# Kernel optimization log

Hardware: AMD Instinct MI355X
Metric: run time of the kernel (lower is better)

## Reference

```python
import jax, jax.numpy as jnp
from jax import lax
import numpy as np

B, T, H, E = 4096, 16, 1024, 1024


def setup_inputs() -> dict:
    key = jax.random.key(0)
    ks = jax.random.split(key, 6)
    query = jax.random.normal(ks[0], (B, H), dtype=jnp.float32)
    topics = jax.random.normal(ks[1], (B, T, E), dtype=jnp.float32)
    coverage_vector = jax.random.uniform(ks[2], (B, T), dtype=jnp.float32)
    # Ua: Linear(embed->hidden, bias=False); weight [H, E]
    Ua_w = jax.random.normal(ks[3], (H, E), dtype=jnp.float32) * 0.03
    # Wa: Linear(hidden->hidden, bias=False). Applied repeatedly (T times) to
    # query in the original loop, so keep spectral norm < 1 for stability.
    Wa_w = jax.random.normal(ks[4], (H, H), dtype=jnp.float32) * 0.01
    # va: Linear(hidden->1, bias=True)
    va_w = jax.random.normal(ks[5], (1, H), dtype=jnp.float32) * 0.03
    va_b = jnp.zeros((1,), dtype=jnp.float32)
    return {"query": query, "topics": topics, "coverage_vector": coverage_vector,
            "Ua_w": Ua_w, "Wa_w": Wa_w, "va_w": va_w, "va_b": va_b}


def reference(query, topics, coverage_vector, Ua_w, Wa_w, va_w, va_b):
    # proj_key for all steps at once: Ua(topics[:, i, :]) -> [B, T, H]
    proj_keys = jnp.einsum('bte,he->bth', topics, Ua_w)
    # Original loop mutates query = Wa(query) each step, so step i uses
    # Wa^(i+1) @ query. Sequential dependence -> lax.scan over T.
    def step(q, pk_c):
        pk, c = pk_c                       # pk: [B, H], c: [B]
        q = q @ Wa_w.T                     # query = Wa(query)
        s = (jnp.tanh(q + pk) @ va_w.T)[:, 0] + va_b[0]  # va(tanh(.)) -> [B]
        return q, s * c                    # scale by coverage C_t[:, i]
    xs = (jnp.swapaxes(proj_keys, 0, 1), coverage_vector.T)  # [T,B,H], [T,B]
    _, scores = lax.scan(step, query, xs)  # scores: [T, B]
    scores = scores.T                      # [B, T]
    alphas = jax.nn.softmax(scores, axis=1)
    mt = jnp.einsum('bt,bte->be', alphas, topics)  # bmm(alphas[:,None,:], topics)
    return mt, alphas
```

## Files before the change

kernel.cpp:

```cpp
#include <hip/hip_runtime.h>

typedef unsigned short u16;
typedef unsigned int u32;
typedef __attribute__((ext_vector_type(8))) __bf16 bf16x8;
typedef __attribute__((ext_vector_type(4))) float f32x4;

__device__ __forceinline__ u16 f2bf(float f) {
  u32 u = __float_as_uint(f);
  u32 r = (u + 0x7FFFu + ((u >> 16) & 1u)) >> 16;
  return (u16)r;
}

__device__ __forceinline__ void gload_lds16(const void* g, void* l) {
  __builtin_amdgcn_global_load_lds((const __attribute__((address_space(1))) u32*)g,
                                   (__attribute__((address_space(3))) u32*)l, 16, 0, 0);
}

__device__ __forceinline__ float fast_tanh(float x) {
  x = fminf(fmaxf(x, -15.f), 15.f);
  float e2 = __expf(2.f * x);
  return (e2 - 1.f) / (e2 + 1.f);
}

__global__ __launch_bounds__(256) void cvt_kernel(const float* __restrict__ src,
                                                  u16* __restrict__ dst, int n4) {
  int stride = gridDim.x * blockDim.x;
  for (int i = blockIdx.x * blockDim.x + threadIdx.x; i < n4; i += stride) {
    float4 v = reinterpret_cast<const float4*>(src)[i];
    ushort4 o;
    o.x = f2bf(v.x); o.y = f2bf(v.y); o.z = f2bf(v.z); o.w = f2bf(v.w);
    reinterpret_cast<ushort4*>(dst)[i] = o;
  }
}

__global__ __launch_bounds__(256) void cvt3t_kernel(const float* __restrict__ q_src, u16* __restrict__ q_dst,
                                                    const float* __restrict__ u_src, u16* __restrict__ u_dst,
                                                    const float* __restrict__ w_src, u16* __restrict__ w_dst,
                                                    u16* __restrict__ wt_dst) {
  __shared__ float tile[32][33];
  int b = blockIdx.x;
  if (b < 6144) {
    const float* src; u16* dst; int i;
    if (b < 4096)      { src = q_src; dst = q_dst; i = b * 256 + threadIdx.x; }
    else if (b < 5120) { src = u_src; dst = u_dst; i = (b - 4096) * 256 + threadIdx.x; }
    else               { src = w_src; dst = w_dst; i = (b - 5120) * 256 + threadIdx.x; }
    float4 v = reinterpret_cast<const float4*>(src)[i];
    ushort4 o;
    o.x = f2bf(v.x); o.y = f2bf(v.y); o.z = f2bf(v.z); o.w = f2bf(v.w);
    reinterpret_cast<ushort4*>(dst)[i] = o;
  } else {
    int tb = b - 6144;
    int tx = threadIdx.x & 31, ty = threadIdx.x >> 5;
    int bx = (tb & 31) * 32, by = (tb >> 5) * 32;
#pragma unroll
    for (int j = 0; j < 32; j += 8)
      tile[ty + j][tx] = w_src[(size_t)(by + ty + j) * 1024 + bx + tx];
    __syncthreads();
#pragma unroll
    for (int j = 0; j < 32; j += 8)
      wt_dst[(size_t)(bx + ty + j) * 1024 + by + tx] = f2bf(tile[tx][ty + j]);
  }
}

__device__ __forceinline__ void stage_tile(const u16* __restrict__ g, size_t row_stride,
                                           u16* lds, int tid) {
#pragma unroll
  for (int s = 0; s < 4; ++s) {
    int chunk = s * 256 + tid;
    int row = chunk >> 3;
    int kcl = (chunk & 7) ^ (row & 7);
    const u16* gp = g + (size_t)row * row_stride + (size_t)(kcl * 8);
    u16* lp = lds + (tid >> 6) * 512 + s * 2048;
    gload_lds16(gp, lp);
  }
}

struct PowArgs {
  const u16* A[8];
  const u16* Bt[8];
  u16* C[8];
  u16* Ct[8];
};

__global__ __launch_bounds__(256) void pow_gemm_kernel(PowArgs args) {
  const u16* A  = args.A[blockIdx.z];
  const u16* Bt = args.Bt[blockIdx.z];
  u16* C  = args.C[blockIdx.z];
  u16* Ct = args.Ct[blockIdx.z];

  __shared__ __align__(16) u16 As[8192];
  __shared__ __align__(16) u16 Bs[8192];

  int tid = threadIdx.x;
  int lane = tid & 63, wave = tid >> 6;
  int wr = wave >> 1, wc = wave & 1;
  int lr = lane & 15, lg = lane >> 4;
  int m0 = blockIdx.x * 128, n0 = blockIdx.y * 128;

  f32x4 acc[4][4];
  const f32x4 zero = {0.f, 0.f, 0.f, 0.f};
#pragma unroll
  for (int m = 0; m < 4; ++m)
#pragma unroll
    for (int n = 0; n < 4; ++n) acc[m][n] = zero;

  for (int k0 = 0; k0 < 1024; k0 += 64) {
    stage_tile(A + (size_t)m0 * 1024 + k0, 1024, As, tid);
    stage_tile(Bt + (size_t)n0 * 1024 + k0, 1024, Bs, tid);
    __syncthreads();
#pragma unroll
    for (int ks = 0; ks < 2; ++ks) {
      bf16x8 a[4], b[4];
#pragma unroll
      for (int m = 0; m < 4; ++m) {
        int ra = wr * 64 + m * 16 + lr;
        a[m] = *reinterpret_cast<const bf16x8*>(As + ra * 64 + (((ks * 4 + lg) ^ (ra & 7)) << 3));
      }
#pragma unroll
      for (int n = 0; n < 4; ++n) {
        int rb = wc * 64 + n * 16 + lr;
        b[n] = *reinterpret_cast<const bf16x8*>(Bs + rb * 64 + (((ks * 4 + lg) ^ (rb & 7)) << 3));
      }
#pragma unroll
      for (int m = 0; m < 4; ++m)
#pragma unroll
        for (int n = 0; n < 4; ++n)
          acc[m][n] = __builtin_amdgcn_mfma_f32_16x16x32_bf16(a[m], b[n], acc[m][n], 0, 0, 0);
    }
    __syncthreads();
  }

#pragma unroll
  for (int m = 0; m < 4; ++m) {
    int row0 = m0 + wr * 64 + m * 16 + lg * 4;
#pragma unroll
    for (int n = 0; n < 4; ++n) {
      int col = n0 + wc * 64 + n * 16 + lr;
      f32x4 c = acc[m][n];
      ushort4 pk;
      pk.x = f2bf(c[0]); pk.y = f2bf(c[1]); pk.z = f2bf(c[2]); pk.w = f2bf(c[3]);
      C[(size_t)(row0 + 0) * 1024 + col] = pk.x;
      C[(size_t)(row0 + 1) * 1024 + col] = pk.y;
      C[(size_t)(row0 + 2) * 1024 + col] = pk.z;
      C[(size_t)(row0 + 3) * 1024 + col] = pk.w;
      *reinterpret_cast<ushort4*>(Ct + (size_t)col * 1024 + row0) = pk;
    }
  }
}

__device__ __forceinline__ void stage_tile64(const u16* __restrict__ g, u16* lds, int tid) {
#pragma unroll
  for (int s = 0; s < 2; ++s) {
    int chunk = s * 256 + tid;
    int row = chunk >> 3;
    int kcl = (chunk & 7) ^ (row & 7);
    const u16* gp = g + (size_t)row * 1024 + (size_t)(kcl * 8);
    u16* lp = lds + (tid >> 6) * 512 + s * 2048;
    gload_lds16(gp, lp);
  }
}

__global__ __launch_bounds__(256) void pow64_gemm_kernel(PowArgs args) {
  const u16* A  = args.A[blockIdx.z];
  const u16* Bt = args.Bt[blockIdx.z];
  u16* C  = args.C[blockIdx.z];
  u16* Ct = args.Ct[blockIdx.z];

  __shared__ __align__(16) u16 As[4096];
  __shared__ __align__(16) u16 Bs[4096];

  int tid = threadIdx.x;
  int lane = tid & 63, wave = tid >> 6;
  int wr = wave >> 1, wc = wave & 1;
  int lr = lane & 15, lg = lane >> 4;
  int m0 = blockIdx.x * 64, n0 = blockIdx.y * 64;

  f32x4 acc[2][2];
  const f32x4 zero = {0.f, 0.f, 0.f, 0.f};
#pragma unroll
  for (int m = 0; m < 2; ++m)
#pragma unroll
    for (int n = 0; n < 2; ++n) acc[m][n] = zero;

  for (int k0 = 0; k0 < 1024; k0 += 64) {
    stage_tile64(A + (size_t)m0 * 1024 + k0, As, tid);
    stage_tile64(Bt + (size_t)n0 * 1024 + k0, Bs, tid);
    __syncthreads();
#pragma unroll
    for (int ks = 0; ks < 2; ++ks) {
      bf16x8 a[2], b[2];
#pragma unroll
      for (int m = 0; m < 2; ++m) {
        int ra = wr * 32 + m * 16 + lr;
        a[m] = *reinterpret_cast<const bf16x8*>(As + ra * 64 + (((ks * 4 + lg) ^ (ra & 7)) << 3));
      }
#pragma unroll
      for (int n = 0; n < 2; ++n) {
        int rb = wc * 32 + n * 16 + lr;
        b[n] = *reinterpret_cast<const bf16x8*>(Bs + rb * 64 + (((ks * 4 + lg) ^ (rb & 7)) << 3));
      }
#pragma unroll
      for (int m = 0; m < 2; ++m)
#pragma unroll
        for (int n = 0; n < 2; ++n)
          acc[m][n] = __builtin_amdgcn_mfma_f32_16x16x32_bf16(a[m], b[n], acc[m][n], 0, 0, 0);
    }
    __syncthreads();
  }

#pragma unroll
  for (int m = 0; m < 2; ++m) {
    int row0 = m0 + wr * 32 + m * 16 + lg * 4;
#pragma unroll
    for (int n = 0; n < 2; ++n) {
      int col = n0 + wc * 32 + n * 16 + lr;
      f32x4 c = acc[m][n];
      ushort4 pk;
      pk.x = f2bf(c[0]); pk.y = f2bf(c[1]); pk.z = f2bf(c[2]); pk.w = f2bf(c[3]);
      C[(size_t)(row0 + 0) * 1024 + col] = pk.x;
      C[(size_t)(row0 + 1) * 1024 + col] = pk.y;
      C[(size_t)(row0 + 2) * 1024 + col] = pk.z;
      C[(size_t)(row0 + 3) * 1024 + col] = pk.w;
      *reinterpret_cast<ushort4*>(Ct + (size_t)col * 1024 + row0) = pk;
    }
  }
}


#define QPHASE(CUR, KS, STAGE_STMT, WAIT_STMT)                                        \
  { _Pragma("unroll") for (int m_ = 0; m_ < 8; ++m_)                                  \
      af[m_] = *reinterpret_cast<const bf16x8*>(lds + aoffv[m_] +                     \
                                                (CUR)*32768 + (KS)*16384);            \
    _Pragma("unroll") for (int n_ = 0; n_ < 4; ++n_)                                  \
      bfr[n_] = *reinterpret_cast<const bf16x8*>(lds + boffv[n_] +                    \
                                                 (CUR)*32768 + (KS)*16384);           \
    STAGE_STMT;                                                                       \
    __builtin_amdgcn_s_barrier();                                                     \
    asm volatile("s_waitcnt lgkmcnt(0)" ::: "memory");                                \
    __builtin_amdgcn_sched_barrier(0);                                                \
    __builtin_amdgcn_s_setprio(1);                                                    \
    _Pragma("unroll") for (int m_ = 0; m_ < 8; ++m_)                                  \
      _Pragma("unroll") for (int n_ = 0; n_ < 4; ++n_)                                \
        acc[m_][n_] =                                                                 \
            __builtin_amdgcn_mfma_f32_16x16x32_bf16(af[m_], bfr[n_], acc[m_][n_], 0, 0, 0); \
    __builtin_amdgcn_s_setprio(0);                                                    \
    WAIT_STMT;                                                                        \
    __builtin_amdgcn_s_barrier();                                                     \
    __builtin_amdgcn_sched_barrier(0); }

__global__ __launch_bounds__(512, 2) void score8_kernel(
    const u16* __restrict__ query_bf, const u16* __restrict__ topics_bf,
    const u16* __restrict__ F_base, const u16* __restrict__ Ua_bf,
    const float* __restrict__ va_w, float* __restrict__ scores_part) {
  extern __shared__ __align__(16) char lds[];

  const int tid = threadIdx.x;
  const int lane = tid & 63, wave = tid >> 6;
  const int wm = wave >> 2, wn = wave & 3;
  const int lr = lane & 15, lg = lane >> 4;

  const int bid = blockIdx.x;
  const int lid = (bid & 7) * 128 + (bid >> 3);
  const int x = lid & 15, y = (lid >> 4) & 3, t = lid >> 6;
  const int m0 = x * 256, n0 = y * 256;
  const int NT = 32;

  const u16* Ft = F_base + (size_t)t * (1024 * 1024);

  u32 aoffv[8], boffv[4];
#pragma unroll
  for (int m = 0; m < 8; ++m) {
    int row = wm * 128 + m * 16 + lr;
    aoffv[m] = row * 64 + ((lg ^ ((row >> 1) & 3)) << 4);
  }
#pragma unroll
  for (int n = 0; n < 4; ++n) {
    int row = wn * 64 + n * 16 + lr;
    boffv[n] = 65536 + row * 64 + ((lg ^ ((row >> 1) & 3)) << 4);
  }

  u32 goff1[2], goff2[2];
#pragma unroll
  for (int s = 0; s < 2; ++s) {
    int c = s * 512 + tid;
    int row = c >> 2;
    int cl = (c & 3) ^ ((row >> 1) & 3);
    goff1[s] = row * 1024 + cl * 8;
    goff2[s] = row * 16384 + cl * 8;
  }
  char* sdst = lds + (tid >> 6) * 1024;
  const u16* qbase = query_bf + (size_t)m0 * 1024;
  const u16* tbase = topics_bf + (size_t)m0 * 16384 + (size_t)t * 1024 - 1024;
  const u16* fbase = Ft + (size_t)n0 * 1024;
  const u16* ubase = Ua_bf + (size_t)n0 * 1024 - 1024;

  auto stageA = [&](int kt, int ks, int buf) {
    const u16* base = (kt < 16 ? qbase : tbase) + kt * 64 + ks * 32;
#pragma unroll
    for (int s = 0; s < 2; ++s) {
      u32 off = (kt < 16) ? goff1[s] : goff2[s];
      gload_lds16(base + off, sdst + buf * 32768 + ks * 16384 + s * 8192);
    }
  };
  auto stageB = [&](int kt, int ks, int buf) {
    const u16* base = (kt < 16 ? fbase : ubase) + kt * 64 + ks * 32;
#pragma unroll
    for (int s = 0; s < 2; ++s)
      gload_lds16(base + goff1[s], sdst + 65536 + buf * 32768 + ks * 16384 + s * 8192);
  };

  f32x4 acc[8][4];
  const f32x4 zero = {0.f, 0.f, 0.f, 0.f};
#pragma unroll
  for (int m = 0; m < 8; ++m)
#pragma unroll
    for (int n = 0; n < 4; ++n) acc[m][n] = zero;

  bf16x8 af[8], bfr[4];

  stageA(0, 0, 0); stageB(0, 0, 0);
  stageA(0, 1, 0); stageB(0, 1, 0);
  stageA(1, 0, 1); stageB(1, 0, 1);
  asm volatile("s_waitcnt vmcnt(4)" ::: "memory");
  __builtin_amdgcn_s_barrier();
  __builtin_amdgcn_sched_barrier(0);

#pragma unroll 2
  for (int kt = 0; kt < NT; ++kt) {
    int cur = kt & 1, nxt = cur ^ 1;
    QPHASE(cur, 0,
           { if (kt + 1 < NT) { stageA(kt + 1, 1, nxt); stageB(kt + 1, 1, nxt); } },
           {});
    QPHASE(cur, 1,
           { if (kt + 2 < NT) { stageA(kt + 2, 0, cur); stageB(kt + 2, 0, cur); } },
           { if (kt < NT - 2)       { asm volatile("s_waitcnt vmcnt(4)" ::: "memory"); }
             else if (kt == NT - 2) { asm volatile("s_waitcnt vmcnt(0)" ::: "memory"); } });
  }

  float va_c[4];
#pragma unroll
  for (int n = 0; n < 4; ++n) va_c[n] = va_w[n0 + wn * 64 + n * 16 + lr];

  float* sred = (float*)lds;
#pragma unroll
  for (int m = 0; m < 8; ++m) {
    float rs[4] = {0.f, 0.f, 0.f, 0.f};
#pragma unroll
    for (int n = 0; n < 4; ++n) {
      f32x4 c = acc[m][n];
      rs[0] += va_c[n] * fast_tanh(c[0]);
      rs[1] += va_c[n] * fast_tanh(c[1]);
      rs[2] += va_c[n] * fast_tanh(c[2]);
      rs[3] += va_c[n] * fast_tanh(c[3]);
    }
#pragma unroll
    for (int j = 0; j < 4; ++j) {
      float v = rs[j];
      v += __shfl_xor(v, 1);
      v += __shfl_xor(v, 2);
      v += __shfl_xor(v, 4);
      v += __shfl_xor(v, 8);
      if (lr == 0) sred[wn * 256 + wm * 128 + m * 16 + lg * 4 + j] = v;
    }
  }
  __syncthreads();
  if (tid < 256) {
    float s = sred[tid] + sred[256 + tid] + sred[512 + tid] + sred[768 + tid];
    scores_part[((size_t)y * 4096 + m0 + tid) * 16 + t] = s;
  }
}

__global__ __launch_bounds__(256) void softmax_mt_kernel(
    const float* __restrict__ scores_part, const float* __restrict__ cov,
    const float* __restrict__ topics, const float* __restrict__ va_b,
    float* __restrict__ mt, float* __restrict__ alphas) {
  int b = blockIdx.x;
  int tid = threadIdx.x;
  float vb = va_b[0];
  float e[16];
  float mx = -3.4e38f;
#pragma unroll
  for (int t = 0; t < 16; ++t) {
    float s = 0.f;
#pragma unroll
    for (int yy = 0; yy < 4; ++yy) s += scores_part[((size_t)yy * 4096 + b) * 16 + t];
    s = (s + vb) * cov[b * 16 + t];
    e[t] = s;
    mx = fmaxf(mx, s);
  }
  float sum = 0.f;
#pragma unroll
  for (int t = 0; t < 16; ++t) { e[t] = __expf(e[t] - mx); sum += e[t]; }
  float inv = 1.f / sum;
  if (tid == 0) {
#pragma unroll
    for (int t = 0; t < 16; ++t) alphas[b * 16 + t] = e[t] * inv;
  }
  const float4* tp = reinterpret_cast<const float4*>(topics + (size_t)b * 16384);
  float4 accv = {0.f, 0.f, 0.f, 0.f};
#pragma unroll
  for (int t = 0; t < 16; ++t) {
    float4 v = tp[t * 256 + tid];
    float a = e[t] * inv;
    accv.x += a * v.x; accv.y += a * v.y; accv.z += a * v.z; accv.w += a * v.w;
  }
  reinterpret_cast<float4*>(mt + (size_t)b * 1024)[tid] = accv;
}

extern "C" void kernel_launch(void* const* d_in, const int* in_sizes, int n_in,
                              void* d_out, int out_size, void* d_ws, size_t ws_size,
                              hipStream_t stream) {
  (void)in_sizes; (void)n_in; (void)out_size; (void)ws_size;
  const float* query = (const float*)d_in[0];
  const float* topics = (const float*)d_in[1];
  const float* cov   = (const float*)d_in[2];
  const float* Ua    = (const float*)d_in[3];
  const float* Wa    = (const float*)d_in[4];
  const float* va_w  = (const float*)d_in[5];
  const float* va_b  = (const float*)d_in[6];

  float* mt = (float*)d_out;
  float* alphas = mt + (size_t)4096 * 1024;

  char* ws = (char*)d_ws;
  u16* topics_bf = (u16*)(ws);
  u16* query_bf  = (u16*)(ws + (size_t)128 * 1024 * 1024);
  u16* Ua_bf     = (u16*)(ws + (size_t)136 * 1024 * 1024);
  u16* F_base    = (u16*)(ws + (size_t)138 * 1024 * 1024);
  u16* FT_base   = (u16*)(ws + (size_t)170 * 1024 * 1024);
  float* scores_part = (float*)(ws + (size_t)202 * 1024 * 1024);

  hipFuncSetAttribute(reinterpret_cast<const void*>(score8_kernel),
                      hipFuncAttributeMaxDynamicSharedMemorySize, 131072);

  cvt_kernel<<<8192, 256, 0, stream>>>(topics, topics_bf, 16777216);
  cvt3t_kernel<<<7168, 256, 0, stream>>>(query, query_bf, Ua, Ua_bf, Wa, F_base, FT_base);

  const size_t MS = 1024 * 1024;
  auto F  = [&](int i) { return F_base + (size_t)i * MS; };
  auto FT = [&](int i) { return FT_base + (size_t)i * MS; };

  PowArgs a1{};
  a1.A[0] = F(0); a1.Bt[0] = FT(0); a1.C[0] = F(1); a1.Ct[0] = FT(1);
  pow64_gemm_kernel<<<dim3(16, 16, 1), 256, 0, stream>>>(a1);
  PowArgs a2{};
  a2.A[0] = F(1); a2.Bt[0] = FT(0); a2.C[0] = F(2); a2.Ct[0] = FT(2);
  a2.A[1] = F(1); a2.Bt[1] = FT(1); a2.C[1] = F(3); a2.Ct[1] = FT(3);
  pow64_gemm_kernel<<<dim3(16, 16, 2), 256, 0, stream>>>(a2);
  PowArgs a3{};
  for (int p = 0; p < 4; ++p) { a3.A[p] = F(3); a3.Bt[p] = FT(p); a3.C[p] = F(4 + p); a3.Ct[p] = FT(4 + p); }
  pow_gemm_kernel<<<dim3(8, 8, 4), 256, 0, stream>>>(a3);
  PowArgs a4{};
  for (int p = 0; p < 8; ++p) { a4.A[p] = F(7); a4.Bt[p] = FT(p); a4.C[p] = F(8 + p); a4.Ct[p] = FT(8 + p); }
  pow_gemm_kernel<<<dim3(8, 8, 8), 256, 0, stream>>>(a4);

  score8_kernel<<<1024, 512, 131072, stream>>>(query_bf, topics_bf, F_base, Ua_bf,
                                               va_w, scores_part);
  softmax_mt_kernel<<<4096, 256, 0, stream>>>(scores_part, cov, topics, va_b, mt, alphas);
}
```

Before: 817.6 us.

## Replace high Wa powers with precomputed q·Wa^8 and reuse low powers

Drops the last batch of eight 1024x1024 matrix-power GEMMs. Instead it computes q8 = query·(Wa^8)^T once with a new qgemm kernel, and score steps 8..15 reuse the powers 0..7 applied to q8. The topics conversion is merged into the other conversion kernels as one launch. The score kernel switches to a 3D grid without the blockIdx swizzle, and setprio/sched_barrier and one barrier are removed from its inner loop. This trades the eight power GEMMs for a single 4096x1024x1024 GEMM. It may hurt the score kernel's scheduling and L2 locality, and it adds one more bf16 rounding step on q8.

After: 792.2 us. 3.1% less time.

```diff
diff --git a/kernel.cpp b/kernel.cpp
--- a/kernel.cpp
+++ b/kernel.cpp
@@ -22,34 +22,32 @@
   return (e2 - 1.f) / (e2 + 1.f);
 }
 
-__global__ __launch_bounds__(256) void cvt_kernel(const float* __restrict__ src,
-                                                  u16* __restrict__ dst, int n4) {
-  int stride = gridDim.x * blockDim.x;
-  for (int i = blockIdx.x * blockDim.x + threadIdx.x; i < n4; i += stride) {
-    float4 v = reinterpret_cast<const float4*>(src)[i];
-    ushort4 o;
-    o.x = f2bf(v.x); o.y = f2bf(v.y); o.z = f2bf(v.z); o.w = f2bf(v.w);
-    reinterpret_cast<ushort4*>(dst)[i] = o;
-  }
-}
-
-__global__ __launch_bounds__(256) void cvt3t_kernel(const float* __restrict__ q_src, u16* __restrict__ q_dst,
-                                                    const float* __restrict__ u_src, u16* __restrict__ u_dst,
-                                                    const float* __restrict__ w_src, u16* __restrict__ w_dst,
-                                                    u16* __restrict__ wt_dst) {
+__global__ __launch_bounds__(256) void cvtall_kernel(
+    const float* __restrict__ topics, u16* __restrict__ topics_bf,
+    const float* __restrict__ q_src, u16* __restrict__ q_dst,
+    const float* __restrict__ u_src, u16* __restrict__ u_dst,
+    const float* __restrict__ w_src, u16* __restrict__ w_dst,
+    u16* __restrict__ wt_dst) {
   __shared__ float tile[32][33];
   int b = blockIdx.x;
-  if (b < 6144) {
+  if (b < 8192) {
+    for (int i = b * 256 + threadIdx.x; i < 16777216; i += 8192 * 256) {
+      float4 v = reinterpret_cast<const float4*>(topics)[i];
+      ushort4 o;
+      o.x = f2bf(v.x); o.y = f2bf(v.y); o.z = f2bf(v.z); o.w = f2bf(v.w);
+      reinterpret_cast<ushort4*>(topics_bf)[i] = o;
+    }
+  } else if (b < 14336) {
     const float* src; u16* dst; int i;
-    if (b < 4096)      { src = q_src; dst = q_dst; i = b * 256 + threadIdx.x; }
-    else if (b < 5120) { src = u_src; dst = u_dst; i = (b - 4096) * 256 + threadIdx.x; }
-    else               { src = w_src; dst = w_dst; i = (b - 5120) * 256 + threadIdx.x; }
+    if (b < 12288)      { src = q_src; dst = q_dst; i = (b - 8192) * 256 + threadIdx.x; }
+    else if (b < 13312) { src = u_src; dst = u_dst; i = (b - 12288) * 256 + threadIdx.x; }
+    else                { src = w_src; dst = w_dst; i = (b - 13312) * 256 + threadIdx.x; }
     float4 v = reinterpret_cast<const float4*>(src)[i];
     ushort4 o;
     o.x = f2bf(v.x); o.y = f2bf(v.y); o.z = f2bf(v.z); o.w = f2bf(v.w);
     reinterpret_cast<ushort4*>(dst)[i] = o;
   } else {
-    int tb = b - 6144;
+    int tb = b - 14336;
     int tx = threadIdx.x & 31, ty = threadIdx.x >> 5;
     int bx = (tb & 31) * 32, by = (tb >> 5) * 32;
 #pragma unroll
@@ -148,6 +146,66 @@
   }
 }
 
+__global__ __launch_bounds__(256) void qgemm_kernel(const u16* __restrict__ A,
+                                                    const u16* __restrict__ Bt,
+                                                    u16* __restrict__ C) {
+  __shared__ __align__(16) u16 As[8192];
+  __shared__ __align__(16) u16 Bs[8192];
+
+  int tid = threadIdx.x;
+  int lane = tid & 63, wave = tid >> 6;
+  int wr = wave >> 1, wc = wave & 1;
+  int lr = lane & 15, lg = lane >> 4;
+  int m0 = blockIdx.x * 128, n0 = blockIdx.y * 128;
+
+  f32x4 acc[4][4];
+  const f32x4 zero = {0.f, 0.f, 0.f, 0.f};
+#pragma unroll
+  for (int m = 0; m < 4; ++m)
+#pragma unroll
+    for (int n = 0; n < 4; ++n) acc[m][n] = zero;
+
+  for (int k0 = 0; k0 < 1024; k0 += 64) {
+    stage_tile(A + (size_t)m0 * 1024 + k0, 1024, As, tid);
+    stage_tile(Bt + (size_t)n0 * 1024 + k0, 1024, Bs, tid);
+    __syncthreads();
+#pragma unroll
+    for (int ks = 0; ks < 2; ++ks) {
+      bf16x8 a[4], b[4];
+#pragma unroll
+      for (int m = 0; m < 4; ++m) {
+        int ra = wr * 64 + m * 16 + lr;
+        a[m] = *reinterpret_cast<const bf16x8*>(As + ra * 64 + (((ks * 4 + lg) ^ (ra & 7)) << 3));
+      }
+#pragma unroll
+      for (int n = 0; n < 4; ++n) {
+        int rb = wc * 64 + n * 16 + lr;
+        b[n] = *reinterpret_cast<const bf16x8*>(Bs + rb * 64 + (((ks * 4 + lg) ^ (rb & 7)) << 3));
+      }
+#pragma unroll
+      for (int m = 0; m < 4; ++m)
+#pragma unroll
+        for (int n = 0; n < 4; ++n)
+          acc[m][n] = __builtin_amdgcn_mfma_f32_16x16x32_bf16(a[m], b[n], acc[m][n], 0, 0, 0);
+    }
+    __syncthreads();
+  }
+
+#pragma unroll
+  for (int m = 0; m < 4; ++m) {
+    int row0 = m0 + wr * 64 + m * 16 + lg * 4;
+#pragma unroll
+    for (int n = 0; n < 4; ++n) {
+      int col = n0 + wc * 64 + n * 16 + lr;
+      f32x4 c = acc[m][n];
+      C[(size_t)(row0 + 0) * 1024 + col] = f2bf(c[0]);
+      C[(size_t)(row0 + 1) * 1024 + col] = f2bf(c[1]);
+      C[(size_t)(row0 + 2) * 1024 + col] = f2bf(c[2]);
+      C[(size_t)(row0 + 3) * 1024 + col] = f2bf(c[3]);
+    }
+  }
+}
+
 __device__ __forceinline__ void stage_tile64(const u16* __restrict__ g, u16* lds, int tid) {
 #pragma unroll
   for (int s = 0; s < 2; ++s) {
@@ -235,21 +293,16 @@
       bfr[n_] = *reinterpret_cast<const bf16x8*>(lds + boffv[n_] +                    \
                                                  (CUR)*32768 + (KS)*16384);           \
     STAGE_STMT;                                                                       \
-    __builtin_amdgcn_s_barrier();                                                     \
-    asm volatile("s_waitcnt lgkmcnt(0)" ::: "memory");                                \
-    __builtin_amdgcn_sched_barrier(0);                                                \
-    __builtin_amdgcn_s_setprio(1);                                                    \
     _Pragma("unroll") for (int m_ = 0; m_ < 8; ++m_)                                  \
       _Pragma("unroll") for (int n_ = 0; n_ < 4; ++n_)                                \
         acc[m_][n_] =                                                                 \
             __builtin_amdgcn_mfma_f32_16x16x32_bf16(af[m_], bfr[n_], acc[m_][n_], 0, 0, 0); \
-    __builtin_amdgcn_s_setprio(0);                                                    \
     WAIT_STMT;                                                                        \
-    __builtin_amdgcn_s_barrier();                                                     \
-    __builtin_amdgcn_sched_barrier(0); }
+    __builtin_amdgcn_s_barrier(); }
 
 __global__ __launch_bounds__(512, 2) void score8_kernel(
-    const u16* __restrict__ query_bf, const u16* __restrict__ topics_bf,
+    const u16* __restrict__ query_bf, const u16* __restrict__ q8_bf,
+    const u16* __restrict__ topics_bf,
     const u16* __restrict__ F_base, const u16* __restrict__ Ua_bf,
     const float* __restrict__ va_w, float* __restrict__ scores_part) {
   extern __shared__ __align__(16) char lds[];
@@ -258,14 +311,11 @@
   const int lane = tid & 63, wave = tid >> 6;
   const int wm = wave >> 2, wn = wave & 3;
   const int lr = lane & 15, lg = lane >> 4;
-
-  const int bid = blockIdx.x;
-  const int lid = (bid & 7) * 128 + (bid >> 3);
-  const int x = lid & 15, y = (lid >> 4) & 3, t = lid >> 6;
-  const int m0 = x * 256, n0 = y * 256;
+  const int m0 = blockIdx.x * 256, n0 = blockIdx.y * 256;
+  const int t = blockIdx.z;
   const int NT = 32;
 
-  const u16* Ft = F_base + (size_t)t * (1024 * 1024);
+  const u16* Ft = F_base + (size_t)(t & 7) * (1024 * 1024);
 
   u32 aoffv[8], boffv[4];
 #pragma unroll
@@ -289,7 +339,7 @@
     goff2[s] = row * 16384 + cl * 8;
   }
   char* sdst = lds + (tid >> 6) * 1024;
-  const u16* qbase = query_bf + (size_t)m0 * 1024;
+  const u16* qbase = (t < 8 ? query_bf : q8_bf) + (size_t)m0 * 1024;
   const u16* tbase = topics_bf + (size_t)m0 * 16384 + (size_t)t * 1024 - 1024;
   const u16* fbase = Ft + (size_t)n0 * 1024;
   const u16* ubase = Ua_bf + (size_t)n0 * 1024 - 1024;
@@ -323,7 +373,6 @@
   stageA(1, 0, 1); stageB(1, 0, 1);
   asm volatile("s_waitcnt vmcnt(4)" ::: "memory");
   __builtin_amdgcn_s_barrier();
-  __builtin_amdgcn_sched_barrier(0);
 
 #pragma unroll 2
   for (int kt = 0; kt < NT; ++kt) {
@@ -366,7 +415,7 @@
   __syncthreads();
   if (tid < 256) {
     float s = sred[tid] + sred[256 + tid] + sred[512 + tid] + sred[768 + tid];
-    scores_part[((size_t)y * 4096 + m0 + tid) * 16 + t] = s;
+    scores_part[((size_t)blockIdx.y * 4096 + m0 + tid) * 16 + t] = s;
   }
 }
 
@@ -427,14 +476,15 @@
   u16* query_bf  = (u16*)(ws + (size_t)128 * 1024 * 1024);
   u16* Ua_bf     = (u16*)(ws + (size_t)136 * 1024 * 1024);
   u16* F_base    = (u16*)(ws + (size_t)138 * 1024 * 1024);
+  u16* q8_bf     = (u16*)(ws + (size_t)154 * 1024 * 1024);
   u16* FT_base   = (u16*)(ws + (size_t)170 * 1024 * 1024);
   float* scores_part = (float*)(ws + (size_t)202 * 1024 * 1024);
 
   hipFuncSetAttribute(reinterpret_cast<const void*>(score8_kernel),
                       hipFuncAttributeMaxDynamicSharedMemorySize, 131072);
 
-  cvt_kernel<<<8192, 256, 0, stream>>>(topics, topics_bf, 16777216);
-  cvt3t_kernel<<<7168, 256, 0, stream>>>(query, query_bf, Ua, Ua_bf, Wa, F_base, FT_base);
+  cvtall_kernel<<<15360, 256, 0, stream>>>(topics, topics_bf, query, query_bf,
+                                           Ua, Ua_bf, Wa, F_base, FT_base);
 
   const size_t MS = 1024 * 1024;
   auto F  = [&](int i) { return F_base + (size_t)i * MS; };
@@ -450,11 +500,10 @@
   PowArgs a3{};
   for (int p = 0; p < 4; ++p) { a3.A[p] = F(3); a3.Bt[p] = FT(p); a3.C[p] = F(4 + p); a3.Ct[p] = FT(4 + p); }
   pow_gemm_kernel<<<dim3(8, 8, 4), 256, 0, stream>>>(a3);
-  PowArgs a4{};
-  for (int p = 0; p < 8; ++p) { a4.A[p] = F(7); a4.Bt[p] = FT(p); a4.C[p] = F(8 + p); a4.Ct[p] = FT(8 + p); }
-  pow_gemm_kernel<<<dim3(8, 8, 8), 256, 0, stream>>>(a4);
-
-  score8_kernel<<<1024, 512, 131072, stream>>>(query_bf, topics_bf, F_base, Ua_bf,
-                                               va_w, scores_part);
+
+  qgemm_kernel<<<dim3(32, 8), 256, 0, stream>>>(query_bf, F(7), q8_bf);
+
+  score8_kernel<<<dim3(16, 4, 16), 512, 131072, stream>>>(query_bf, q8_bf, topics_bf,
+                                                          F_base, Ua_bf, va_w, scores_part);
   softmax_mt_kernel<<<4096, 256, 0, stream>>>(scores_part, cov, topics, va_b, mt, alphas);
 }
```
